# Kernel optimization log

Measured on AMD Instinct MI355X. Metric: run time of the kernel, lower is better.

The kernel has to match this reference:

```python
import jax, jax.numpy as jnp
import numpy as np

D_MODEL = 1024
NHEAD = 16
D_K = D_MODEL // NHEAD


def setup_inputs() -> dict:
    key = jax.random.key(0)
    ks = jax.random.split(key, 12)
    B, L = 4, 2048
    s = 1.0 / np.sqrt(D_MODEL)
    inp = {
        "query": jax.random.normal(ks[0], (B, L, D_MODEL), jnp.float32),
        "key": jax.random.normal(ks[1], (B, L, D_MODEL), jnp.float32),
        "value": jax.random.normal(ks[2], (B, L, D_MODEL), jnp.float32),
        "Wq": jax.random.normal(ks[3], (D_MODEL, D_MODEL), jnp.float32) * s,
        "bq": jnp.zeros((D_MODEL,), jnp.float32),
        "Wk": jax.random.normal(ks[4], (D_MODEL, D_MODEL), jnp.float32) * s,
        "bk": jnp.zeros((D_MODEL,), jnp.float32),
        "Wv": jax.random.normal(ks[5], (D_MODEL, D_MODEL), jnp.float32) * s,
        "bv": jnp.zeros((D_MODEL,), jnp.float32),
        "Wo": jax.random.normal(ks[6], (D_MODEL, D_MODEL), jnp.float32) * s,
        "bo": jnp.zeros((D_MODEL,), jnp.float32),
    }
    return inp


def reference(query, key, value, Wq, bq, Wk, bk, Wv, bv, Wo, bo):
    B, Lq, _ = query.shape
    Lk = key.shape[1]
    # Linear projections, split into heads: [B, H, L, d_k]
    Q = (query @ Wq + bq).reshape(B, Lq, NHEAD, D_K).transpose(0, 2, 1, 3)
    K = (key @ Wk + bk).reshape(B, Lk, NHEAD, D_K).transpose(0, 2, 1, 3)
    V = (value @ Wv + bv).reshape(B, Lk, NHEAD, D_K).transpose(0, 2, 1, 3)
    scale = 1.0 / jnp.sqrt(jnp.asarray(D_K, Q.dtype))
    scores = jnp.einsum("bhqd,bhkd->bhqk", Q, K) * scale  # [B,H,Lq,Lk]
    attn = jax.nn.softmax(scores, axis=-1)
    context = jnp.einsum("bhqk,bhkd->bhqd", attn, V)
    context = context.transpose(0, 2, 1, 3).reshape(B, Lq, D_MODEL)
    return context @ Wo + bo
```

## Files before the change

kernel.cpp:

```cpp
#include <hip/hip_runtime.h>
#include <hip/hip_bf16.h>
#include <cstdint>
#include <cstddef>


typedef unsigned short u16;
typedef __bf16 bf8v __attribute__((ext_vector_type(8)));
typedef __bf16 bf4v __attribute__((ext_vector_type(4)));
typedef float f32x4 __attribute__((ext_vector_type(4)));

#define D_MODEL 1024
#define NHEAD   16
#define DK      64
#define BATCH   4
#define SEQ     2048
#define ROWS    (BATCH * SEQ)

__device__ __forceinline__ u16 f2b(float f) {
  union { float f; unsigned int i; } x; x.f = f;
  unsigned int r = x.i + 0x7fffu + ((x.i >> 16) & 1u);
  return (u16)(r >> 16);
}
__device__ __forceinline__ ushort4 pack4(float a, float b, float c, float d) {
  union { bf4v v; ushort4 u; } x;
  x.v[0] = (__bf16)a; x.v[1] = (__bf16)b; x.v[2] = (__bf16)c; x.v[3] = (__bf16)d;
  return x.u;
}
__device__ __forceinline__ void async16(const void* g, void* l) {
  __builtin_amdgcn_global_load_lds((const __attribute__((address_space(1))) void*)g,
                                   (__attribute__((address_space(3))) void*)l, 16, 0, 0);
}
#define MFMA16(a, b, c) __builtin_amdgcn_mfma_f32_16x16x32_bf16(a, b, c, 0, 0, 0)

__global__ void wtrans_cvt_kernel(const float* __restrict__ w0, const float* __restrict__ w1,
                                  const float* __restrict__ w2, const float* __restrict__ w3,
                                  u16* __restrict__ dst4) {
  __shared__ float t[32][33];
  const float* src = (blockIdx.z == 0) ? w0 : (blockIdx.z == 1) ? w1
                   : (blockIdx.z == 2) ? w2 : w3;
  u16* dst = dst4 + (size_t)blockIdx.z * D_MODEL * D_MODEL;
  const int c0 = blockIdx.x * 32, r0 = blockIdx.y * 32;
  for (int i = threadIdx.y; i < 32; i += 8)
    t[i][threadIdx.x] = src[(size_t)(r0 + i) * D_MODEL + c0 + threadIdx.x];
  __syncthreads();
  for (int i = threadIdx.y; i < 32; i += 8)
    dst[(size_t)(c0 + i) * D_MODEL + r0 + threadIdx.x] = f2b(t[threadIdx.x][i]);
}

__global__ __launch_bounds__(256) void cvt_f2b_kernel(const float* __restrict__ src,
                                                      u16* __restrict__ dst, int n4) {
  const int i = blockIdx.x * 256 + threadIdx.x;
  if (i < n4) {
    const float4 v = ((const float4*)src)[i];
    ushort4 o;
    o.x = f2b(v.x); o.y = f2b(v.y); o.z = f2b(v.z); o.w = f2b(v.w);
    ((ushort4*)dst)[i] = o;
  }
}

#define BM 64
#define BN 128
#define BK 32

__global__ __launch_bounds__(256) void gemm_bt(const u16* __restrict__ A,
                                               const u16* __restrict__ Bt,
                                               const float* __restrict__ bias,
                                               void* __restrict__ out, int mode,
                                               float oscale) {
  __shared__ __align__(16) u16 As[BM * BK];
  __shared__ __align__(16) u16 Bs[BN * BK];
  const int tid = threadIdx.x;
  const int lane = tid & 63, wave = tid >> 6;
  const int wm = wave >> 1, wn = wave & 1;
  const int quad = lane >> 4, l16 = lane & 15;
  const int m0 = blockIdx.x * BM, n0 = blockIdx.y * BN;
  const int K = 1024;

  f32x4 acc[2][4];
#pragma unroll
  for (int i = 0; i < 2; i++)
#pragma unroll
    for (int j = 0; j < 4; j++) acc[i][j] = (f32x4){0.f, 0.f, 0.f, 0.f};

  const int srow = tid >> 2;
  const int sch = ((tid & 3) ^ ((tid >> 3) & 3)) * 8;
  const int fsw = (quad ^ ((l16 >> 1) & 3)) * 8;
  const u16* Ag = A + (size_t)(m0 + srow) * K + sch;
  const u16* Bg = Bt + (size_t)(n0 + srow) * K + sch;

  for (int k0 = 0; k0 < K; k0 += BK) {
    async16(Ag + k0, &As[tid * 8]);
    async16(Bg + k0, &Bs[tid * 8]);
    async16(Bg + (size_t)64 * K + k0, &Bs[2048 + tid * 8]);
    __syncthreads();

    bf8v af[2], bfr[4];
#pragma unroll
    for (int i = 0; i < 2; i++)
      af[i] = *(const bf8v*)&As[(wm * 32 + i * 16 + l16) * BK + fsw];
#pragma unroll
    for (int j = 0; j < 4; j++)
      bfr[j] = *(const bf8v*)&Bs[(wn * 64 + j * 16 + l16) * BK + fsw];
#pragma unroll
    for (int i = 0; i < 2; i++)
#pragma unroll
      for (int j = 0; j < 4; j++)
        acc[i][j] = MFMA16(af[i], bfr[j], acc[i][j]);
    __syncthreads();
  }

#pragma unroll
  for (int j = 0; j < 4; j++) {
    const int n = n0 + wn * 64 + j * 16 + l16;
    const float bv = bias[n];
#pragma unroll
    for (int i = 0; i < 2; i++) {
      const int gr0 = m0 + wm * 32 + i * 16 + quad * 4;
#pragma unroll
      for (int r = 0; r < 4; r++) {
        const int row = gr0 + r;
        const float val = (acc[i][j][r] + bv) * oscale;
        if (mode == 2) {
          ((float*)out)[(size_t)row * D_MODEL + n] = val;
        } else {
          const int b = row >> 11, l = row & 2047;
          const int h = n >> 6, d = n & 63;
          if (mode == 0) {
            ((u16*)out)[(((size_t)(b * NHEAD + h) * SEQ + l) << 6) + d] = f2b(val);
          } else {
            const int pl = (l & ~31) | ((l & 12) << 1) | ((l & 16) >> 2) | (l & 3);
            ((u16*)out)[(((size_t)(b * NHEAD + h) * DK + d) << 11) + pl] = f2b(val);
          }
        }
      }
    }
  }
}

__global__ __launch_bounds__(256, 4) void attn_kernel(const u16* __restrict__ Q,
                                                      const u16* __restrict__ K,
                                                      const u16* __restrict__ Vt,
                                                      u16* __restrict__ ctx) {
  const int bh = blockIdx.x;
  const int qb = blockIdx.y * 128;
  const int tid = threadIdx.x;
  const int lane = tid & 63, wave = tid >> 6;
  const int quad = lane >> 4, l16 = lane & 15;
  const u16* Qh = Q + (size_t)bh * SEQ * DK;
  const u16* Kh = K + (size_t)bh * SEQ * DK;
  const u16* Vh = Vt + (size_t)bh * DK * SEQ;

  __shared__ __align__(16) u16 Ks[2][2][64 * 32];
  __shared__ __align__(16) u16 Vs[2][64 * 64];

  const int srow = tid >> 2;
  const int sch  = ((tid & 3) ^ ((tid >> 3) & 3)) * 8;
  const int ldst = tid * 8;
  const int fsw  = (quad ^ ((l16 >> 1) & 3)) * 8;
  const int vd   = tid >> 3;
  const int vcol = ((tid & 7) ^ ((tid >> 3) & 7)) * 8;

  bf8v qf[2][2];
#pragma unroll
  for (int qg = 0; qg < 2; qg++)
#pragma unroll
    for (int h = 0; h < 2; h++)
      qf[qg][h] = *(const bf8v*)&Qh[(size_t)(qb + wave * 32 + qg * 16 + l16) * DK + h * 32 + quad * 8];

  bf8v ones;
#pragma unroll
  for (int j = 0; j < 8; j++) ones[j] = (__bf16)1.0f;

  f32x4 o[2][4];
  f32x4 la[2];
  float m_q[2];
#pragma unroll
  for (int qg = 0; qg < 2; qg++) {
    m_q[qg] = -1e30f; la[qg] = (f32x4){0.f, 0.f, 0.f, 0.f};
#pragma unroll
    for (int d = 0; d < 4; d++) o[qg][d] = (f32x4){0.f, 0.f, 0.f, 0.f};
  }

  async16(Kh + (size_t)srow * DK + sch,      &Ks[0][0][ldst]);
  async16(Kh + (size_t)srow * DK + 32 + sch, &Ks[0][1][ldst]);
  async16(Vh + (size_t)vd * SEQ + vcol,        &Vs[0][ldst]);
  async16(Vh + (size_t)(vd + 32) * SEQ + vcol, &Vs[0][2048 + ldst]);
  __syncthreads();

  int p = 0;
  for (int kt = 0; kt < SEQ; kt += 64) {
    const int nt = kt + 64;
    if (nt < SEQ) {
      async16(Kh + (size_t)(nt + srow) * DK + sch,      &Ks[p ^ 1][0][ldst]);
      async16(Kh + (size_t)(nt + srow) * DK + 32 + sch, &Ks[p ^ 1][1][ldst]);
      async16(Vh + (size_t)vd * SEQ + nt + vcol,        &Vs[p ^ 1][ldst]);
      async16(Vh + (size_t)(vd + 32) * SEQ + nt + vcol, &Vs[p ^ 1][2048 + ldst]);
    }

    bf8v kf[4][2];
#pragma unroll
    for (int nb = 0; nb < 4; nb++)
#pragma unroll
      for (int h = 0; h < 2; h++)
        kf[nb][h] = *(const bf8v*)&Ks[p][h][(nb * 16 + l16) * 32 + fsw];

    bf8v pf[2][2];
#pragma unroll
    for (int qg = 0; qg < 2; qg++) {
      f32x4 s[4];
      __builtin_amdgcn_s_setprio(1);
#pragma unroll
      for (int nb = 0; nb < 4; nb++) {
        f32x4 t = (f32x4){0.f, 0.f, 0.f, 0.f};
        t = MFMA16(kf[nb][0], qf[qg][0], t);
        t = MFMA16(kf[nb][1], qf[qg][1], t);
        s[nb] = t;
      }
      __builtin_amdgcn_s_setprio(0);
      float t0 = fmaxf(fmaxf(s[0][0], s[0][1]), fmaxf(s[0][2], s[0][3]));
      float t1 = fmaxf(fmaxf(s[1][0], s[1][1]), fmaxf(s[1][2], s[1][3]));
      float t2 = fmaxf(fmaxf(s[2][0], s[2][1]), fmaxf(s[2][2], s[2][3]));
      float t3 = fmaxf(fmaxf(s[3][0], s[3][1]), fmaxf(s[3][2], s[3][3]));
      float mx = fmaxf(fmaxf(t0, t1), fmaxf(t2, t3));
      mx = fmaxf(mx, __shfl_xor(mx, 16));
      mx = fmaxf(mx, __shfl_xor(mx, 32));
      const float mprev = m_q[qg];
      float Mn = mprev;
      const int resc = !__all(mx - mprev <= 8.0f);
      if (resc) {
        Mn = fmaxf(mprev, mx);
        const float al = __builtin_amdgcn_exp2f(mprev - Mn);
        m_q[qg] = Mn;
        la[qg] *= al;
#pragma unroll
        for (int d = 0; d < 4; d++) o[qg][d] *= al;
      }
#pragma unroll
      for (int nb = 0; nb < 4; nb++)
#pragma unroll
        for (int r = 0; r < 4; r++)
          s[nb][r] = __builtin_amdgcn_exp2f(s[nb][r] - Mn);
#pragma unroll
      for (int kc = 0; kc < 2; kc++) {
        bf8v pw;
#pragma unroll
        for (int j = 0; j < 4; j++) {
          pw[j]     = (__bf16)s[2 * kc][j];
          pw[j + 4] = (__bf16)s[2 * kc + 1][j];
        }
        pf[qg][kc] = pw;
      }
      la[qg] = MFMA16(ones, pf[qg][0], la[qg]);
      la[qg] = MFMA16(ones, pf[qg][1], la[qg]);
    }

    bf8v vf[4][2];
#pragma unroll
    for (int dc = 0; dc < 4; dc++) {
      const int rb = (dc * 16 + l16) * 64;
#pragma unroll
      for (int kc = 0; kc < 2; kc++)
        vf[dc][kc] = *(const bf8v*)&Vs[p][rb + (((kc * 4 + quad) ^ (l16 & 7)) * 8)];
    }
    __builtin_amdgcn_s_setprio(1);
#pragma unroll
    for (int qg = 0; qg < 2; qg++)
#pragma unroll
      for (int dc = 0; dc < 4; dc++) {
        o[qg][dc] = MFMA16(vf[dc][0], pf[qg][0], o[qg][dc]);
        o[qg][dc] = MFMA16(vf[dc][1], pf[qg][1], o[qg][dc]);
      }
    __builtin_amdgcn_s_setprio(0);

    __syncthreads();
    p ^= 1;
  }

  const int b = bh >> 4, hh = bh & 15;
#pragma unroll
  for (int qg = 0; qg < 2; qg++) {
    const float inv = __builtin_amdgcn_rcpf(la[qg][0]);
    const int q = qb + wave * 32 + qg * 16 + l16;
#pragma unroll
    for (int dc = 0; dc < 4; dc++) {
      const int col = hh * 64 + dc * 16 + quad * 4;
      *(ushort4*)&ctx[(size_t)(b * SEQ + q) * D_MODEL + col] =
          pack4(o[qg][dc][0] * inv, o[qg][dc][1] * inv,
                o[qg][dc][2] * inv, o[qg][dc][3] * inv);
    }
  }
}

extern "C" void kernel_launch(void* const* d_in, const int* in_sizes, int n_in,
                              void* d_out, int out_size, void* d_ws, size_t ws_size,
                              hipStream_t stream) {
  const float* q  = (const float*)d_in[0];
  const float* k  = (const float*)d_in[1];
  const float* v  = (const float*)d_in[2];
  const float* Wq = (const float*)d_in[3];
  const float* bq = (const float*)d_in[4];
  const float* Wk = (const float*)d_in[5];
  const float* bk = (const float*)d_in[6];
  const float* Wv = (const float*)d_in[7];
  const float* bv = (const float*)d_in[8];
  const float* Wo = (const float*)d_in[9];
  const float* bo = (const float*)d_in[10];

  u16* ws  = (u16*)d_ws;
  u16* wt  = ws;
  u16* act = wt + (size_t)4 * D_MODEL * D_MODEL;
  u16* Qw  = act + (size_t)ROWS * D_MODEL;
  u16* Kw  = Qw + (size_t)ROWS * D_MODEL;
  u16* Vt  = Kw + (size_t)ROWS * D_MODEL;

  const int n4 = ROWS * D_MODEL / 4;
  dim3 gg(ROWS / BM, D_MODEL / BN), gb(256);
  const float QSCALE = 0.18033688011112042f;

  wtrans_cvt_kernel<<<dim3(32, 32, 4), dim3(32, 8), 0, stream>>>(Wq, Wk, Wv, Wo, wt);

  cvt_f2b_kernel<<<n4 / 256, 256, 0, stream>>>(q, act, n4);
  gemm_bt<<<gg, gb, 0, stream>>>(act, wt,                                 bq, Qw, 0, QSCALE);
  cvt_f2b_kernel<<<n4 / 256, 256, 0, stream>>>(k, act, n4);
  gemm_bt<<<gg, gb, 0, stream>>>(act, wt + (size_t)1 * D_MODEL * D_MODEL, bk, Kw, 0, 1.0f);
  cvt_f2b_kernel<<<n4 / 256, 256, 0, stream>>>(v, act, n4);
  gemm_bt<<<gg, gb, 0, stream>>>(act, wt + (size_t)2 * D_MODEL * D_MODEL, bv, Vt, 1, 1.0f);

  attn_kernel<<<dim3(BATCH * NHEAD, SEQ / 128), 256, 0, stream>>>(Qw, Kw, Vt, act);

  gemm_bt<<<gg, gb, 0, stream>>>(act, wt + (size_t)3 * D_MODEL * D_MODEL, bo, d_out, 2, 1.0f);
}
```

Before: 390.9 us.

## Fuse fp32-to-bf16 conversion into a batched QKV GEMM with larger tiles

```diff
diff --git a/kernel.cpp b/kernel.cpp
--- a/kernel.cpp
+++ b/kernel.cpp
@@ -25,6 +25,12 @@
   union { bf4v v; ushort4 u; } x;
   x.v[0] = (__bf16)a; x.v[1] = (__bf16)b; x.v[2] = (__bf16)c; x.v[3] = (__bf16)d;
   return x.u;
+}
+__device__ __forceinline__ bf8v cvt8(float4 a, float4 b) {
+  bf8v r;
+  r[0] = (__bf16)a.x; r[1] = (__bf16)a.y; r[2] = (__bf16)a.z; r[3] = (__bf16)a.w;
+  r[4] = (__bf16)b.x; r[5] = (__bf16)b.y; r[6] = (__bf16)b.z; r[7] = (__bf16)b.w;
+  return r;
 }
 __device__ __forceinline__ void async16(const void* g, void* l) {
   __builtin_amdgcn_global_load_lds((const __attribute__((address_space(1))) void*)g,
@@ -47,38 +53,143 @@
     dst[(size_t)(c0 + i) * D_MODEL + r0 + threadIdx.x] = f2b(t[threadIdx.x][i]);
 }
 
-__global__ __launch_bounds__(256) void cvt_f2b_kernel(const float* __restrict__ src,
-                                                      u16* __restrict__ dst, int n4) {
-  const int i = blockIdx.x * 256 + threadIdx.x;
-  if (i < n4) {
-    const float4 v = ((const float4*)src)[i];
-    ushort4 o;
-    o.x = f2b(v.x); o.y = f2b(v.y); o.z = f2b(v.z); o.w = f2b(v.w);
-    ((ushort4*)dst)[i] = o;
-  }
-}
-
-#define BM 64
+#define BM 128
 #define BN 128
 #define BK 32
 
-__global__ __launch_bounds__(256) void gemm_bt(const u16* __restrict__ A,
-                                               const u16* __restrict__ Bt,
-                                               const float* __restrict__ bias,
-                                               void* __restrict__ out, int mode,
-                                               float oscale) {
+__global__ __launch_bounds__(256) void gemm_qkv(
+    const float* __restrict__ Aq, const float* __restrict__ Ak,
+    const float* __restrict__ Av, const u16* __restrict__ wt,
+    const float* __restrict__ bq, const float* __restrict__ bk,
+    const float* __restrict__ bv, u16* __restrict__ Qw, u16* __restrict__ Kw,
+    u16* __restrict__ Vt, float qscale) {
   __shared__ __align__(16) u16 As[BM * BK];
   __shared__ __align__(16) u16 Bs[BN * BK];
+  const int z = blockIdx.y;
+  const float* A = (z == 0) ? Aq : (z == 1) ? Ak : Av;
+  const u16* Bt = wt + (size_t)z * D_MODEL * D_MODEL;
+  const float* bias = (z == 0) ? bq : (z == 1) ? bk : bv;
+  u16* out = (z == 0) ? Qw : (z == 1) ? Kw : Vt;
+  const float oscale = (z == 0) ? qscale : 1.0f;
+
+  const int lid = blockIdx.x;
+  const int xcd = lid & 7, jj = lid >> 3;
+  const int m0 = ((xcd << 3) + (jj >> 3)) * BM;
+  const int n0 = (jj & 7) * BN;
+
   const int tid = threadIdx.x;
   const int lane = tid & 63, wave = tid >> 6;
   const int wm = wave >> 1, wn = wave & 1;
   const int quad = lane >> 4, l16 = lane & 15;
-  const int m0 = blockIdx.x * BM, n0 = blockIdx.y * BN;
   const int K = 1024;
 
-  f32x4 acc[2][4];
-#pragma unroll
-  for (int i = 0; i < 2; i++)
+  f32x4 acc[4][4];
+#pragma unroll
+  for (int i = 0; i < 4; i++)
+#pragma unroll
+    for (int j = 0; j < 4; j++) acc[i][j] = (f32x4){0.f, 0.f, 0.f, 0.f};
+
+  const int srow = tid >> 2;
+  const int sch = ((tid & 3) ^ ((tid >> 3) & 3)) * 8;
+  const int fsw = (quad ^ ((l16 >> 1) & 3)) * 8;
+  const float* Ag0 = A + (size_t)(m0 + srow) * K + sch;
+  const float* Ag1 = Ag0 + (size_t)64 * K;
+  const u16* Bg = Bt + (size_t)(n0 + srow) * K + sch;
+
+  float4 ar0 = *(const float4*)(Ag0);
+  float4 ar1 = *(const float4*)(Ag0 + 4);
+  float4 ar2 = *(const float4*)(Ag1);
+  float4 ar3 = *(const float4*)(Ag1 + 4);
+
+  for (int k0 = 0; k0 < K; k0 += BK) {
+    async16(Bg + k0, &Bs[tid * 8]);
+    async16(Bg + (size_t)64 * K + k0, &Bs[2048 + tid * 8]);
+    *(bf8v*)&As[tid * 8]        = cvt8(ar0, ar1);
+    *(bf8v*)&As[2048 + tid * 8] = cvt8(ar2, ar3);
+    __syncthreads();
+    if (k0 + BK < K) {
+      ar0 = *(const float4*)(Ag0 + k0 + BK);
+      ar1 = *(const float4*)(Ag0 + k0 + BK + 4);
+      ar2 = *(const float4*)(Ag1 + k0 + BK);
+      ar3 = *(const float4*)(Ag1 + k0 + BK + 4);
+    }
+
+    bf8v af[4], bfr[4];
+#pragma unroll
+    for (int i = 0; i < 4; i++)
+      af[i] = *(const bf8v*)&As[(wm * 64 + i * 16 + l16) * BK + fsw];
+#pragma unroll
+    for (int j = 0; j < 4; j++)
+      bfr[j] = *(const bf8v*)&Bs[(wn * 64 + j * 16 + l16) * BK + fsw];
+    if (z < 2) {
+#pragma unroll
+      for (int i = 0; i < 4; i++)
+#pragma unroll
+        for (int j = 0; j < 4; j++)
+          acc[i][j] = MFMA16(bfr[j], af[i], acc[i][j]);
+    } else {
+#pragma unroll
+      for (int i = 0; i < 4; i++)
+#pragma unroll
+        for (int j = 0; j < 4; j++)
+          acc[i][j] = MFMA16(af[i], bfr[j], acc[i][j]);
+    }
+    __syncthreads();
+  }
+
+  if (z < 2) {
+#pragma unroll
+    for (int i = 0; i < 4; i++) {
+      const int m = m0 + wm * 64 + i * 16 + l16;
+      const int b = m >> 11, l = m & 2047;
+#pragma unroll
+      for (int j = 0; j < 4; j++) {
+        const int n = n0 + wn * 64 + j * 16 + quad * 4;
+        const float4 bv4 = *(const float4*)&bias[n];
+        const int h = n >> 6, d = n & 63;
+        *(ushort4*)&out[(((size_t)(b * NHEAD + h) * SEQ + l) << 6) + d] =
+            pack4((acc[i][j][0] + bv4.x) * oscale, (acc[i][j][1] + bv4.y) * oscale,
+                  (acc[i][j][2] + bv4.z) * oscale, (acc[i][j][3] + bv4.w) * oscale);
+      }
+    }
+  } else {
+#pragma unroll
+    for (int j = 0; j < 4; j++) {
+      const int n = n0 + wn * 64 + j * 16 + l16;
+      const float bvs = bias[n];
+      const int h = n >> 6, d = n & 63;
+#pragma unroll
+      for (int i = 0; i < 4; i++) {
+        const int row = m0 + wm * 64 + i * 16 + quad * 4;
+        const int b = row >> 11, l = row & 2047;
+        const int pl = (l & ~31) | ((l & 12) << 1) | ((l & 16) >> 2);
+        *(ushort4*)&out[(((size_t)(b * NHEAD + h) * DK + d) << 11) + pl] =
+            pack4(acc[i][j][0] + bvs, acc[i][j][1] + bvs,
+                  acc[i][j][2] + bvs, acc[i][j][3] + bvs);
+      }
+    }
+  }
+}
+
+__global__ __launch_bounds__(256) void gemm_out(const u16* __restrict__ A,
+                                                const u16* __restrict__ Bt,
+                                                const float* __restrict__ bias,
+                                                float* __restrict__ out) {
+  __shared__ __align__(16) u16 As[BM * BK];
+  __shared__ __align__(16) u16 Bs[BN * BK];
+  const int lid = blockIdx.x;
+  const int xcd = lid & 7, jj = lid >> 3;
+  const int m0 = ((xcd << 3) + (jj >> 3)) * BM;
+  const int n0 = (jj & 7) * BN;
+  const int tid = threadIdx.x;
+  const int lane = tid & 63, wave = tid >> 6;
+  const int wm = wave >> 1, wn = wave & 1;
+  const int quad = lane >> 4, l16 = lane & 15;
+  const int K = 1024;
+
+  f32x4 acc[4][4];
+#pragma unroll
+  for (int i = 0; i < 4; i++)
 #pragma unroll
     for (int j = 0; j < 4; j++) acc[i][j] = (f32x4){0.f, 0.f, 0.f, 0.f};
 
@@ -90,49 +201,37 @@
 
   for (int k0 = 0; k0 < K; k0 += BK) {
     async16(Ag + k0, &As[tid * 8]);
+    async16(Ag + (size_t)64 * K + k0, &As[2048 + tid * 8]);
     async16(Bg + k0, &Bs[tid * 8]);
     async16(Bg + (size_t)64 * K + k0, &Bs[2048 + tid * 8]);
     __syncthreads();
 
-    bf8v af[2], bfr[4];
-#pragma unroll
-    for (int i = 0; i < 2; i++)
-      af[i] = *(const bf8v*)&As[(wm * 32 + i * 16 + l16) * BK + fsw];
+    bf8v af[4], bfr[4];
+#pragma unroll
+    for (int i = 0; i < 4; i++)
+      af[i] = *(const bf8v*)&As[(wm * 64 + i * 16 + l16) * BK + fsw];
 #pragma unroll
     for (int j = 0; j < 4; j++)
       bfr[j] = *(const bf8v*)&Bs[(wn * 64 + j * 16 + l16) * BK + fsw];
 #pragma unroll
-    for (int i = 0; i < 2; i++)
+    for (int i = 0; i < 4; i++)
 #pragma unroll
       for (int j = 0; j < 4; j++)
-        acc[i][j] = MFMA16(af[i], bfr[j], acc[i][j]);
+        acc[i][j] = MFMA16(bfr[j], af[i], acc[i][j]);
     __syncthreads();
   }
 
 #pragma unroll
-  for (int j = 0; j < 4; j++) {
-    const int n = n0 + wn * 64 + j * 16 + l16;
-    const float bv = bias[n];
-#pragma unroll
-    for (int i = 0; i < 2; i++) {
-      const int gr0 = m0 + wm * 32 + i * 16 + quad * 4;
-#pragma unroll
-      for (int r = 0; r < 4; r++) {
-        const int row = gr0 + r;
-        const float val = (acc[i][j][r] + bv) * oscale;
-        if (mode == 2) {
-          ((float*)out)[(size_t)row * D_MODEL + n] = val;
-        } else {
-          const int b = row >> 11, l = row & 2047;
-          const int h = n >> 6, d = n & 63;
-          if (mode == 0) {
-            ((u16*)out)[(((size_t)(b * NHEAD + h) * SEQ + l) << 6) + d] = f2b(val);
-          } else {
-            const int pl = (l & ~31) | ((l & 12) << 1) | ((l & 16) >> 2) | (l & 3);
-            ((u16*)out)[(((size_t)(b * NHEAD + h) * DK + d) << 11) + pl] = f2b(val);
-          }
-        }
-      }
+  for (int i = 0; i < 4; i++) {
+    const int m = m0 + wm * 64 + i * 16 + l16;
+#pragma unroll
+    for (int j = 0; j < 4; j++) {
+      const int n = n0 + wn * 64 + j * 16 + quad * 4;
+      const float4 bv4 = *(const float4*)&bias[n];
+      float4 vv;
+      vv.x = acc[i][j][0] + bv4.x; vv.y = acc[i][j][1] + bv4.y;
+      vv.z = acc[i][j][2] + bv4.z; vv.w = acc[i][j][3] + bv4.w;
+      *(float4*)&out[(size_t)m * D_MODEL + n] = vv;
     }
   }
 }
@@ -308,25 +407,19 @@
 
   u16* ws  = (u16*)d_ws;
   u16* wt  = ws;
-  u16* act = wt + (size_t)4 * D_MODEL * D_MODEL;
-  u16* Qw  = act + (size_t)ROWS * D_MODEL;
+  u16* Qw  = wt + (size_t)4 * D_MODEL * D_MODEL;
   u16* Kw  = Qw + (size_t)ROWS * D_MODEL;
   u16* Vt  = Kw + (size_t)ROWS * D_MODEL;
-
-  const int n4 = ROWS * D_MODEL / 4;
-  dim3 gg(ROWS / BM, D_MODEL / BN), gb(256);
+  u16* ctx = Vt + (size_t)ROWS * D_MODEL;
+
   const float QSCALE = 0.18033688011112042f;
 
   wtrans_cvt_kernel<<<dim3(32, 32, 4), dim3(32, 8), 0, stream>>>(Wq, Wk, Wv, Wo, wt);
 
-  cvt_f2b_kernel<<<n4 / 256, 256, 0, stream>>>(q, act, n4);
-  gemm_bt<<<gg, gb, 0, stream>>>(act, wt,                                 bq, Qw, 0, QSCALE);
-  cvt_f2b_kernel<<<n4 / 256, 256, 0, stream>>>(k, act, n4);
-  gemm_bt<<<gg, gb, 0, stream>>>(act, wt + (size_t)1 * D_MODEL * D_MODEL, bk, Kw, 0, 1.0f);
-  cvt_f2b_kernel<<<n4 / 256, 256, 0, stream>>>(v, act, n4);
-  gemm_bt<<<gg, gb, 0, stream>>>(act, wt + (size_t)2 * D_MODEL * D_MODEL, bv, Vt, 1, 1.0f);
-
-  attn_kernel<<<dim3(BATCH * NHEAD, SEQ / 128), 256, 0, stream>>>(Qw, Kw, Vt, act);
-
-  gemm_bt<<<gg, gb, 0, stream>>>(act, wt + (size_t)3 * D_MODEL * D_MODEL, bo, d_out, 2, 1.0f);
-}
+  gemm_qkv<<<dim3(512, 3), 256, 0, stream>>>(q, k, v, wt, bq, bk, bv, Qw, Kw, Vt, QSCALE);
+
+  attn_kernel<<<dim3(BATCH * NHEAD, SEQ / 128), 256, 0, stream>>>(Qw, Kw, Vt, ctx);
+
+  gemm_out<<<512, 256, 0, stream>>>(ctx, wt + (size_t)3 * D_MODEL * D_MODEL, bo,
+                                    (float*)d_out);
+}
```

Result: faster. 378.4 us (-3.2%).
